# Performance work log

Hardware: AMD Instinct MI355X
Metric: run time of the kernel (lower is better)

## Reference

```python
import jax, jax.numpy as jnp
import numpy as np

B, V = 128, 128000
NEG_INF = float('-inf')


def _apply_top_k(logits, top_ks):
    vocab = logits.shape[-1]
    valid_k = jnp.where(top_ks > 0, jnp.minimum(top_ks, vocab), vocab)  # [B]
    order = jnp.argsort(-logits, axis=-1)                 # descending sort indices [B,V]
    sorted_logits = jnp.take_along_axis(logits, order, axis=-1)
    ranks = jnp.arange(vocab)[None, :]                    # [1,V]
    keep = ranks < valid_k[:, None]
    masked_sorted = jnp.where(keep, sorted_logits, NEG_INF)
    rows = jnp.arange(logits.shape[0])[:, None]
    return jnp.zeros_like(logits).at[rows, order].set(masked_sorted)


def _apply_top_p(logits, top_ps):
    order = jnp.argsort(-logits, axis=-1)
    sorted_logits = jnp.take_along_axis(logits, order, axis=-1)
    sorted_probs = jax.nn.softmax(sorted_logits, axis=-1)
    cum = jnp.cumsum(sorted_probs, axis=-1)
    keep = cum < top_ps[:, None]
    keep = keep.at[:, 0].set(True)                        # always keep the top token
    masked_sorted = jnp.where(keep, sorted_logits, NEG_INF)
    rows = jnp.arange(logits.shape[0])[:, None]
    return jnp.zeros_like(logits).at[rows, order].set(masked_sorted)


def setup_inputs() -> dict:
    key = jax.random.key(0)
    k1, k2, k3, k4, k5 = jax.random.split(key, 5)
    logits = jax.random.normal(k1, (B, V), dtype=jnp.float32) * 4.0
    temperatures = jax.random.uniform(k2, (B,), dtype=jnp.float32) + 0.5  # [0.5, 1.5)
    top_ks = jax.random.randint(k3, (B,), 0, 100, dtype=jnp.int64)        # 0 -> disabled
    top_ps = jax.random.uniform(k4, (B,), dtype=jnp.float32)
    # uniform noise; reference converts to Exp(1) via -log(u)
    exp_noise_u = jax.random.uniform(k5, (B, V), dtype=jnp.float32, minval=1e-12, maxval=1.0)
    return {"logits": logits, "temperatures": temperatures, "top_ks": top_ks,
            "top_ps": top_ps, "exp_noise_u": exp_noise_u}


def reference(logits, temperatures, top_ks, top_ps, exp_noise_u):
    x = logits.astype(jnp.float32) / temperatures[:, None]
    x = _apply_top_k(x, top_ks)
    x = _apply_top_p(x, top_ps)
    probs = jax.nn.softmax(x, axis=-1)
    q = jnp.clip(-jnp.log(exp_noise_u), 1e-10)            # Exp(1) samples, clamped like torch
    sample_tokens = jnp.argmax(probs / q, axis=-1)
    return sample_tokens
```

## Files before the change

### kernel.cpp

```cpp
#include <hip/hip_runtime.h>
#include <math.h>

#define SA 8
#define SEG2 8
#define NB 4096
#define TAA 512
#define HS 256
#define TE 512
#define TBB 1024
#define SCT 256
#define CH (NB / SCT)
#define CAPSEG 512
#define GTOT (SA * CAPSEG)
#define MAXM1 16
#define GB1 16384
#define SUBC 512
#define EQC 64
#define FXS 1099511627776.0f
#define FXI (1.0f / 1099511627776.0f)

typedef unsigned u32;
typedef unsigned long long u64;

struct ScanSh {
  u32 axc[SCT]; float axe[SCT];
  u32 sufc[SCT]; float sufe[SCT];
  int cbin[SCT]; u32 cca[SCT]; float cea[SCT];
  int fbin[SCT]; u32 fca[SCT]; float fea[SCT];
};

__device__ __forceinline__ u32 f2key(float f) {
  u32 u = __float_as_uint(f);
  return u ^ ((u >> 31) ? 0xFFFFFFFFu : 0x80000000u);
}
__device__ __forceinline__ int is_mode0(int k, int V) {
  return (k >= 1 && k <= 256 && k < V);
}

__device__ int m1_slot(const int* topks, int row, int V, int tid, int* red) {
  if (tid < 128) {
    int c = 0;
    for (int r = tid; r < row; r += 128) c += !is_mode0(topks[r], V);
    red[tid] = c;
  }
  __syncthreads();
  for (int s = 64; s > 0; s >>= 1) {
    if (tid < s) red[tid] += red[tid + s];
    __syncthreads();
  }
  return red[0];
}

__device__ __forceinline__ float row_max(const float* maxpart, int row) {
  float mm = maxpart[row * SA];
  for (int j = 1; j < SA; ++j) mm = fmaxf(mm, maxpart[row * SA + j]);
  return mm;
}

__device__ void scan_level(const u32* cnt, const u64* e0, ScanSh* ax,
                           u32* sprefix, int* scnt_above, float* sexp_above,
                           float target, int tid) {
  if (tid < SCT) {
    u32 cc = 0; float ce = 0.f; const int base = tid * CH;
    for (int j = 0; j < CH; ++j) { cc += cnt[base + j]; ce += (float)e0[base + j] * FXI; }
    ax->axc[tid] = cc; ax->axe[tid] = ce;
  }
  __syncthreads();
  if (tid == 0) {
    u32 rc = 0; float re = 0.f;
    for (int c = SCT - 1; c >= 0; --c) {
      ax->sufc[c] = rc; ax->sufe[c] = re;
      rc += ax->axc[c]; re += ax->axe[c];
    }
  }
  __syncthreads();
  if (tid < SCT) {
    const int base = tid * CH;
    u32 rc = ax->sufc[tid]; float re = ax->sufe[tid];
    int best = -1; u32 bca = 0; float bea = 0.f;
    int fb = -1; u32 ffca = 0; float ffea = 0.f;
    for (int b = base + CH - 1; b >= base; --b) {
      u32 c = cnt[b]; float ebv = (float)e0[b] * FXI;
      bool cross = (c > 0) && ((re + ebv) >= target);
      if (cross && best < 0) { best = b; bca = rc; bea = re; }
      if (c > 0) { fb = b; ffca = rc; ffea = re; }
      rc += c; re += ebv;
    }
    ax->cbin[tid] = best; ax->cca[tid] = bca; ax->cea[tid] = bea;
    ax->fbin[tid] = fb; ax->fca[tid] = ffca; ax->fea[tid] = ffea;
  }
  __syncthreads();
  if (tid == 0) {
    int bsel = -1; u32 ca = 0; float ea = 0.f;
    for (int c = 0; c < SCT; ++c) {
      int b = ax->cbin[c];
      if (b > bsel) { bsel = b; ca = ax->cca[c]; ea = ax->cea[c]; }
    }
    if (bsel < 0) {
      for (int c = 0; c < SCT; ++c) {
        int b = ax->fbin[c];
        if (b >= 0 && (bsel < 0 || b < bsel)) { bsel = b; ca = ax->fca[c]; ea = ax->fea[c]; }
      }
    }
    if (bsel < 0) bsel = 0;
    *sprefix = (u32)bsel;
    *scnt_above = (int)ca;
    *sexp_above = ea;
  }
  __syncthreads();
}

__global__ __launch_bounds__(TAA) void kA(const float* __restrict__ logits,
                                          const float* __restrict__ temps,
                                          const int* __restrict__ topks,
                                          float* __restrict__ maxpart,
                                          u32* __restrict__ scnt,
                                          float* __restrict__ candv,
                                          int* __restrict__ candi, int V) {
  const int row = blockIdx.x, seg = blockIdx.y, tid = threadIdx.x;
  __shared__ u32 cnt[NB];
  __shared__ float sm[TAA];
  __shared__ u32 cs[HS];
  __shared__ int bb[HS];
  __shared__ int lcnt;
  __shared__ u32 sT;
  const int k = topks[row];
  const int m0 = is_mode0(k, V);
  const float t = temps[row];
  const float* lr = logits + (size_t)row * V;
  const float4* l4 = (const float4*)lr;
  const int n4 = V >> 2;
  const int q0 = (int)((long long)seg * n4 / SA);
  const int q1 = (int)((long long)(seg + 1) * n4 / SA);
  float mx = -INFINITY;
  if (m0) {
    for (int i = tid; i < NB; i += TAA) cnt[i] = 0;
    if (tid == 0) lcnt = 0;
    __syncthreads();
    for (int i = q0 + tid; i < q1; i += TAA) {
      float4 v = l4[i];
      float xs[4] = {v.x / t, v.y / t, v.z / t, v.w / t};
#pragma unroll
      for (int j = 0; j < 4; ++j) {
        mx = fmaxf(mx, xs[j]);
        atomicAdd(&cnt[f2key(xs[j]) >> 20], 1u);
      }
    }
    if (seg == SA - 1)
      for (int i = (n4 << 2) + tid; i < V; i += TAA) {
        float x = lr[i] / t;
        mx = fmaxf(mx, x);
        atomicAdd(&cnt[f2key(x) >> 20], 1u);
      }
  } else {
    for (int i = q0 + tid; i < q1; i += TAA) {
      float4 v = l4[i];
      mx = fmaxf(mx, fmaxf(fmaxf(v.x, v.y), fmaxf(v.z, v.w)) / t);
    }
    if (seg == SA - 1)
      for (int i = (n4 << 2) + tid; i < V; i += TAA) mx = fmaxf(mx, lr[i] / t);
  }
  sm[tid] = mx;
  __syncthreads();
  for (int s = TAA >> 1; s > 0; s >>= 1) {
    if (tid < s) sm[tid] = fmaxf(sm[tid], sm[tid + s]);
    __syncthreads();
  }
  if (tid == 0) maxpart[row * SA + seg] = sm[0];
  if (!m0) return;
  if (tid < HS) {
    u32 cc = 0; const int base = tid * (NB / HS);
    for (int j = 0; j < NB / HS; ++j) cc += cnt[base + j];
    cs[tid] = cc;
  }
  __syncthreads();
  if (tid == 0) {
    u32 rc = 0;
    for (int c = HS - 1; c >= 0; --c) { u32 tmp = cs[c]; cs[c] = rc; rc += tmp; }
  }
  __syncthreads();
  const int kk = (k > 256) ? 256 : k;
  if (tid < HS) {
    const int base = tid * (NB / HS);
    u32 rc = cs[tid]; int best = -1;
    for (int b = base + NB / HS - 1; b >= base; --b) {
      u32 c = cnt[b];
      if (c && best < 0 && (int)(rc + c) >= kk) best = b;
      rc += c;
    }
    bb[tid] = best;
  }
  __syncthreads();
  if (tid == 0) {
    int bsel = -1;
    for (int c = 0; c < HS; ++c) if (bb[c] > bsel) bsel = bb[c];
    if (bsel < 0) { for (int b = 0; b < NB; ++b) if (cnt[b]) { bsel = b; break; } }
    if (bsel < 0) bsel = 0;
    sT = ((u32)bsel) << 20;
  }
  __syncthreads();
  const u32 T = sT;
  const size_t cbase = ((size_t)row * SA + seg) * CAPSEG;
  for (int i = q0 + tid; i < q1; i += TAA) {
    float4 v = l4[i];
    float xs[4] = {v.x / t, v.y / t, v.z / t, v.w / t};
#pragma unroll
    for (int j = 0; j < 4; ++j) {
      if (f2key(xs[j]) >= T) {
        int s = atomicAdd(&lcnt, 1);
        if (s < CAPSEG) { candv[cbase + s] = xs[j]; candi[cbase + s] = i * 4 + j; }
      }
    }
  }
  if (seg == SA - 1)
    for (int i = (n4 << 2) + tid; i < V; i += TAA) {
      float x = lr[i] / t;
      if (f2key(x) >= T) {
        int s = atomicAdd(&lcnt, 1);
        if (s < CAPSEG) { candv[cbase + s] = x; candi[cbase + s] = i; }
      }
    }
  __syncthreads();
  if (tid == 0) { int n = lcnt; if (n > CAPSEG) n = CAPSEG; scnt[row * SA + seg] = (u32)n; }
}

__global__ __launch_bounds__(TE) void kE(const float* __restrict__ logits,
                                         const float* __restrict__ temps,
                                         const int* __restrict__ topks,
                                         const float* __restrict__ maxpart,
                                         float* __restrict__ Sparts,
                                         u32* __restrict__ m1c0,
                                         u64* __restrict__ m1e0, int V) {
  const int row = blockIdx.x, seg = blockIdx.y, tid = threadIdx.x;
  const int k = topks[row];
  if (is_mode0(k, V)) return;
  __shared__ int red[128];
  const int slot = m1_slot(topks, row, V, tid, red);
  if (slot >= MAXM1) return;
  __shared__ u32 c0[NB];
  __shared__ u64 e0[NB];
  __shared__ float ss[TE];
  for (int i = tid; i < NB; i += TE) { c0[i] = 0; e0[i] = 0ull; }
  __syncthreads();
  const float t = temps[row];
  const float m = row_max(maxpart, row);
  const float* lr = logits + (size_t)row * V;
  const float4* l4 = (const float4*)lr;
  const int n4 = V >> 2;
  const int q0 = (int)((long long)seg * n4 / SEG2);
  const int q1 = (int)((long long)(seg + 1) * n4 / SEG2);
  float ls = 0.f;
  for (int i = q0 + tid; i < q1; i += TE) {
    float4 v = l4[i];
    float xs[4] = {v.x / t, v.y / t, v.z / t, v.w / t};
#pragma unroll
    for (int j = 0; j < 4; ++j) {
      float e = expf(xs[j] - m);
      ls += e;
      u32 b = f2key(xs[j]) >> 20;
      atomicAdd(&c0[b], 1u);
      u64 fx = (u64)(e * FXS);
      if (fx) atomicAdd(&e0[b], fx);
    }
  }
  if (seg == SEG2 - 1)
    for (int i = (n4 << 2) + tid; i < V; i += TE) {
      float x = lr[i] / t;
      float e = expf(x - m);
      ls += e;
      u32 b = f2key(x) >> 20;
      atomicAdd(&c0[b], 1u);
      u64 fx = (u64)(e * FXS);
      if (fx) atomicAdd(&e0[b], fx);
    }
  ss[tid] = ls;
  __syncthreads();
  for (int s = TE >> 1; s > 0; s >>= 1) {
    if (tid < s) ss[tid] += ss[tid + s];
    __syncthreads();
  }
  if (tid == 0) Sparts[slot * SEG2 + seg] = ss[0];
  for (int b = tid; b < NB; b += TE) {
    u32 c = c0[b]; if (c) atomicAdd(&m1c0[(size_t)slot * NB + b], c);
    u64 e = e0[b]; if (e) atomicAdd(&m1e0[(size_t)slot * NB + b], e);
  }
}

__global__ __launch_bounds__(TBB) void kM1(const float* __restrict__ logits,
                                           const float* __restrict__ temps,
                                           const int* __restrict__ topks,
                                           const float* __restrict__ topps,
                                           const float* __restrict__ noise,
                                           const float* __restrict__ maxpart,
                                           const float* __restrict__ Sparts,
                                           const u32* __restrict__ m1c0,
                                           const u64* __restrict__ m1e0,
                                           u64* __restrict__ g1p,
                                           u32* __restrict__ gcnt,
                                           u64* __restrict__ rpack,
                                           u32* __restrict__ rdone,
                                           int* __restrict__ out, int V) {
  const int row = blockIdx.x, seg = blockIdx.y, tid = threadIdx.x;
  const int k = topks[row];
  if (is_mode0(k, V)) return;
  __shared__ int red[128];
  const int slot = m1_slot(topks, row, V, tid, red);
  if (slot >= MAXM1) return;

  __shared__ u32 cnt[NB];
  __shared__ u64 e0[NB];
  __shared__ ScanSh ax;
  __shared__ u32 spfx; __shared__ int sca; __shared__ float sea;
  __shared__ float rr[TBB]; __shared__ int ri[TBB];
  for (int i = tid; i < NB; i += TBB) {
    cnt[i] = m1c0[(size_t)slot * NB + i];
    e0[i] = m1e0[(size_t)slot * NB + i];
  }
  __syncthreads();
  float S = 0.f;
  for (int j = 0; j < SEG2; ++j) S += Sparts[slot * SEG2 + j];
  const float target = topps[row] * S;
  scan_level(cnt, e0, &ax, &spfx, &sca, &sea, target, tid);
  const u32 pfx = spfx;

  const float t = temps[row];
  const float m = row_max(maxpart, row);
  const float* lr = logits + (size_t)row * V;
  const float* ur = noise + (size_t)row * V;
  const float4* l4 = (const float4*)lr;
  const float4* u4 = (const float4*)ur;
  const int n4 = V >> 2;
  const int q0 = (int)((long long)seg * n4 / SEG2);
  const int q1 = (int)((long long)(seg + 1) * n4 / SEG2);
  const size_t gbase = (size_t)slot * GB1;

  float best = -1.f; int bidx = 0x7FFFFFFF;
  for (int i = q0 + tid; i < q1; i += TBB) {
    float4 xv = l4[i];
    float4 uv = u4[i];
    float xs[4] = {xv.x / t, xv.y / t, xv.z / t, xv.w / t};
    float us[4] = {uv.x, uv.y, uv.z, uv.w};
#pragma unroll
    for (int j = 0; j < 4; ++j) {
      u32 key = f2key(xs[j]);
      u32 bin = key >> 20;
      int idx = i * 4 + j;
      if (bin == pfx) {
        u32 s2 = atomicAdd(&gcnt[slot], 1u);
        if (s2 < GB1)
          atomicExch(&g1p[gbase + s2],
                     ((u64)__float_as_uint(xs[j]) << 32) | (u64)(u32)idx);
      } else if (bin > pfx) {
        float q = fmaxf(-logf(us[j]), 1e-10f);
        float rt = expf(xs[j] - m) / q;
        if (rt > best || (rt == best && idx < bidx)) { best = rt; bidx = idx; }
      }
    }
  }
  if (seg == SEG2 - 1)
    for (int i = (n4 << 2) + tid; i < V; i += TBB) {
      float x = lr[i] / t;
      u32 key = f2key(x);
      u32 bin = key >> 20;
      if (bin == pfx) {
        u32 s2 = atomicAdd(&gcnt[slot], 1u);
        if (s2 < GB1)
          atomicExch(&g1p[gbase + s2],
                     ((u64)__float_as_uint(x) << 32) | (u64)(u32)i);
      } else if (bin > pfx) {
        float q = fmaxf(-logf(ur[i]), 1e-10f);
        float rt = expf(x - m) / q;
        if (rt > best || (rt == best && i < bidx)) { best = rt; bidx = i; }
      }
    }
  rr[tid] = best; ri[tid] = bidx;
  __syncthreads();
  for (int s = TBB >> 1; s > 0; s >>= 1) {
    if (tid < s) {
      float ov = rr[tid + s]; int oi = ri[tid + s];
      if (ov > rr[tid] || (ov == rr[tid] && oi < ri[tid])) { rr[tid] = ov; ri[tid] = oi; }
    }
    __syncthreads();
  }
  __shared__ int slast;
  if (tid == 0) {
    if (rr[0] >= 0.f) {
      u64 pk = ((u64)f2key(rr[0]) << 32) | (u64)(0xFFFFFFFFu - (u32)ri[0]);
      atomicMax(&rpack[row], pk);
    }
    __threadfence();
    u32 arr = atomicAdd(&rdone[row], 1u);
    slast = (arr == (u32)(SEG2 - 1)) ? 1 : 0;
  }
  __syncthreads();
  if (!slast) return;
  __threadfence();

  __shared__ u32 cnt1[1024]; __shared__ u64 fx1[1024];
  __shared__ u32 csuf[1024]; __shared__ u64 esuf[1024];
  __shared__ float subv[SUBC]; __shared__ int subi[SUBC];
  __shared__ float ssv[SUBC]; __shared__ int ssi[SUBC];
  __shared__ int eqs[EQC];
  __shared__ int scross, sfb, sca1, sns, seqn;
  __shared__ float sea1; __shared__ u32 svstar;

  int nf = (int)atomicAdd(&gcnt[slot], 0u);
  if (nf > GB1) nf = GB1;
  cnt1[tid] = 0; fx1[tid] = 0ull;
  if (tid == 0) { sns = 0; scross = -1; sfb = 0x7FFFFFFF; }
  __syncthreads();
  for (int i = tid; i < nf; i += TBB) {
    u64 p = atomicAdd(&g1p[gbase + i], 0ull);
    float x = __uint_as_float((u32)(p >> 32));
    u32 b = (f2key(x) >> 10) & 0x3FFu;
    float e = expf(x - m);
    atomicAdd(&cnt1[b], 1u);
    u64 fx = (u64)(e * FXS);
    if (fx) atomicAdd(&fx1[b], fx);
  }
  __syncthreads();
  csuf[tid] = cnt1[tid]; esuf[tid] = fx1[tid];
  __syncthreads();
  for (int stp = 1; stp < 1024; stp <<= 1) {
    u32 ca_ = 0; u64 ea_ = 0ull;
    if (tid + stp < 1024) { ca_ = csuf[tid + stp]; ea_ = esuf[tid + stp]; }
    __syncthreads();
    csuf[tid] += ca_; esuf[tid] += ea_;
    __syncthreads();
  }
  {
    u32 c = cnt1[tid];
    if (c) {
      float racc = (float)(esuf[tid] - fx1[tid]) * FXI;
      float ebv = (float)fx1[tid] * FXI;
      if (sea + (racc + ebv) >= target) atomicMax(&scross, tid);
      atomicMin(&sfb, tid);
    }
  }
  __syncthreads();
  if (tid == 0) {
    int cb = scross;
    if (cb < 0) cb = (sfb != 0x7FFFFFFF) ? sfb : 0;
    u32 cAbove = csuf[cb] - cnt1[cb];
    float eAbove = (float)(esuf[cb] - fx1[cb]) * FXI;
    scross = cb;
    sea1 = sea + eAbove;
    sca1 = sca + (int)cAbove;
  }
  __syncthreads();
  const u32 cb = (u32)scross;
  for (int i = tid; i < nf; i += TBB) {
    u64 p = atomicAdd(&g1p[gbase + i], 0ull);
    float x = __uint_as_float((u32)(p >> 32));
    if (((f2key(x) >> 10) & 0x3FFu) == cb) {
      int s2 = atomicAdd(&sns, 1);
      if (s2 < SUBC) { subv[s2] = x; subi[s2] = (int)(u32)(p & 0xFFFFFFFFull); }
    }
  }
  __syncthreads();
  int ns = sns; if (ns > SUBC) ns = SUBC;
  for (int i = tid; i < ns; i += TBB) {
    float v = subv[i]; int ix = subi[i];
    int rank = 0;
    for (int j2 = 0; j2 < ns; ++j2) {
      float vj = subv[j2]; int ij = subi[j2];
      if (vj > v || (vj == v && ij < ix)) rank++;
    }
    ssv[rank] = v; ssi[rank] = ix;
  }
  __syncthreads();
  if (tid == 0) {
    const float p = topps[row];
    float run_n = sea1 / S;
    const int have_above = (sca1 > 0);
    u32 lastkey = 0u; int lastr = 0, laststart = -1, anykept = 0;
    u32 vsel = 0u; int rsel = -1, bstart = 0;
    int j = 0;
    while (j < ns) {
      u32 key = f2key(ssv[j]);
      int c = 1;
      while (j + c < ns && f2key(ssv[j + c]) == key) ++c;
      float e = expf(ssv[j] - m);
      float en = e / S;
      int kept = 0;
      for (int q = 0; q < c; ++q) {
        float nn = run_n + en;
        if (nn < p) { run_n = nn; kept++; } else break;
      }
      if (kept == c) { lastkey = key; lastr = c; laststart = j; anykept = 1; j += c; continue; }
      if (kept > 0) { vsel = key; rsel = kept; bstart = j; }
      else if (anykept) { vsel = lastkey; rsel = lastr; bstart = laststart; }
      else if (have_above) { vsel = key; rsel = 0; bstart = j; }
      else { vsel = key; rsel = 1; bstart = j; }
      break;
    }
    if (rsel < 0) {
      if (anykept) { vsel = lastkey; rsel = lastr; bstart = laststart; }
      else if (ns > 0) {
        vsel = f2key(ssv[0]); bstart = 0;
        rsel = have_above ? 0 : 1;
      } else { vsel = 0u; rsel = 0; bstart = 0; }
    }
    int eqn = rsel;
    if (eqn > EQC) eqn = EQC;
    if (eqn < 0) eqn = 0;
    if (bstart + eqn > ns) eqn = ns - bstart;
    if (eqn < 0) eqn = 0;
    for (int q2 = 0; q2 < eqn; ++q2) eqs[q2] = ssi[bstart + q2];
    seqn = eqn; svstar = vsel;
  }
  __syncthreads();

  const u32 vk = svstar;
  const int eqn = seqn;
  best = -1.f; bidx = 0x7FFFFFFF;
  for (int i = tid; i < nf; i += TBB) {
    u64 p = atomicAdd(&g1p[gbase + i], 0ull);
    float x = __uint_as_float((u32)(p >> 32));
    int ix = (int)(u32)(p & 0xFFFFFFFFull);
    u32 key = f2key(x);
    bool kept = key > vk;
    if (!kept && key == vk) {
      for (int e = 0; e < eqn; ++e) if (eqs[e] == ix) { kept = true; break; }
    }
    if (kept) {
      float q = fmaxf(-logf(ur[ix]), 1e-10f);
      float rt = expf(x - m) / q;
      if (rt > best || (rt == best && ix < bidx)) { best = rt; bidx = ix; }
    }
  }
  rr[tid] = best; ri[tid] = bidx;
  __syncthreads();
  for (int s = TBB >> 1; s > 0; s >>= 1) {
    if (tid < s) {
      float ov = rr[tid + s]; int oi = ri[tid + s];
      if (ov > rr[tid] || (ov == rr[tid] && oi < ri[tid])) { rr[tid] = ov; ri[tid] = oi; }
    }
    __syncthreads();
  }
  if (tid == 0) {
    u64 myPk = 0ull;
    if (rr[0] >= 0.f)
      myPk = ((u64)f2key(rr[0]) << 32) | (u64)(0xFFFFFFFFu - (u32)ri[0]);
    u64 prev = atomicMax(&rpack[row], myPk);
    u64 fin = prev > myPk ? prev : myPk;
    out[row] = (int)(0xFFFFFFFFu - (u32)(fin & 0xFFFFFFFFull));
  }
}

__global__ __launch_bounds__(TBB) void kH(const float* __restrict__ topps,
                                          const float* __restrict__ noise,
                                          const int* __restrict__ topks,
                                          const float* __restrict__ maxpart,
                                          const u32* __restrict__ scnt,
                                          const float* __restrict__ candv,
                                          const int* __restrict__ candi,
                                          int* __restrict__ out, int V) {
  const int row = blockIdx.x, tid = threadIdx.x;
  const int kR = topks[row];
  if (!is_mode0(kR, V)) return;
  __shared__ float gv[GTOT]; __shared__ int gi[GTOT];
  __shared__ float sv[CAPSEG]; __shared__ int si[CAPSEG];
  __shared__ float fv[CAPSEG]; __shared__ int fi[CAPSEG];
  __shared__ float pe[CAPSEG];
  __shared__ float rr[TBB]; __shared__ int ri[TBB];
  __shared__ int offs[SA + 1];
  __shared__ u32 dh[256]; __shared__ u32 dsufx[256];
  __shared__ u32 sPrefix; __shared__ int sRemain, sNf, sDig;
  __shared__ int sJ; __shared__ float sZ2;
  if (tid == 0) {
    int o = 0;
    for (int s = 0; s < SA; ++s) {
      offs[s] = o;
      int c = (int)scnt[row * SA + s];
      if (c > CAPSEG) c = CAPSEG;
      if (c < 0) c = 0;
      o += c;
    }
    offs[SA] = o;
  }
  __syncthreads();
  const int g = offs[SA];
  for (int s = 0; s < SA; ++s) {
    const int o = offs[s], c = offs[s + 1] - o;
    const size_t cbase = ((size_t)row * SA + s) * CAPSEG;
    for (int i = tid; i < c; i += TBB) { gv[o + i] = candv[cbase + i]; gi[o + i] = candi[cbase + i]; }
  }
  __syncthreads();
  int kk = kR; if (kk > 256) kk = 256; if (kk > g) kk = g;
  if (tid == 0) { sPrefix = 0u; sRemain = (kk < 1) ? 1 : kk; }
  __syncthreads();
  for (int pass = 0; pass < 4; ++pass) {
    const int shift = 24 - 8 * pass;
    if (tid < 256) dh[tid] = 0;
    if (tid == 0) sDig = -1;
    __syncthreads();
    const u32 pref = sPrefix;
    for (int i = tid; i < g; i += TBB) {
      u32 key = f2key(gv[i]);
      if (pass == 0 || (key >> (shift + 8)) == pref)
        atomicAdd(&dh[(key >> shift) & 0xFFu], 1u);
    }
    __syncthreads();
    if (tid < 256) dsufx[tid] = dh[tid];
    __syncthreads();
    for (int stp = 1; stp < 256; stp <<= 1) {
      u32 addv = 0;
      if (tid < 256 && tid + stp < 256) addv = dsufx[tid + stp];
      __syncthreads();
      if (tid < 256) dsufx[tid] += addv;
      __syncthreads();
    }
    if (tid < 256) {
      u32 excl = dsufx[tid] - dh[tid];
      u32 rem = (u32)sRemain;
      if (dh[tid] && excl < rem && excl + dh[tid] >= rem) sDig = tid;
    }
    __syncthreads();
    if (tid == 0) {
      int d = sDig; if (d < 0) d = 0;
      u32 excl = dsufx[d] - dh[d];
      sRemain -= (int)excl;
      sPrefix = (sPrefix << 8) | (u32)d;
      if (pass == 3) sNf = 0;
    }
    __syncthreads();
  }
  const u32 Tk = sPrefix;
  for (int i = tid; i < g; i += TBB) {
    if (f2key(gv[i]) >= Tk) {
      int s = atomicAdd(&sNf, 1);
      if (s < CAPSEG) { fv[s] = gv[i]; fi[s] = gi[i]; }
    }
  }
  __syncthreads();
  int nf = sNf; if (nf > CAPSEG) nf = CAPSEG;
  for (int i = tid; i < nf; i += TBB) {
    float v = fv[i]; int ix = fi[i];
    int rank = 0;
    for (int j = 0; j < nf; ++j) {
      float vj = fv[j]; int ij = fi[j];
      if (vj > v || (vj == v && ij < ix)) rank++;
    }
    sv[rank] = v; si[rank] = ix;
  }
  __syncthreads();
  const float m = row_max(maxpart, row);
  const float p = topps[row];
  int keff = kR; if (keff > nf) keff = nf;
  for (int j = tid; j < keff; j += TBB) pe[j] = expf(sv[j] - m);
  __syncthreads();
  if (tid == 0) {
    int J = 1; float Z2 = 1.f;
    if (nf > 0 && keff > 0) {
      float Zk = 0.f;
      for (int j = 0; j < keff; ++j) Zk += pe[j];
      float c = 0.f; int Jc = 0;
      for (int j = 0; j < keff; ++j) {
        float pr = pe[j] / Zk;
        c += pr;
        if (c < p) Jc++;
      }
      if (Jc < 1) Jc = 1;
      J = Jc;
      Z2 = 0.f;
      for (int j = 0; j < J && j < keff; ++j) Z2 += pe[j];
    }
    sJ = J; sZ2 = Z2;
  }
  __syncthreads();
  const int J = sJ; const float Z2 = sZ2;
  float best = -1.f; int bidx = 0x7FFFFFFF;
  for (int j = tid; j < J && j < nf; j += TBB) {
    int ix = si[j];
    float u = noise[(size_t)row * V + ix];
    float q = fmaxf(-logf(u), 1e-10f);
    float pr = pe[j] / Z2;
    float rt = pr / q;
    if (rt > best || (rt == best && ix < bidx)) { best = rt; bidx = ix; }
  }
  rr[tid] = best; ri[tid] = bidx;
  __syncthreads();
  for (int s = TBB >> 1; s > 0; s >>= 1) {
    if (tid < s) {
      float ov = rr[tid + s]; int oi = ri[tid + s];
      if (ov > rr[tid] || (ov == rr[tid] && oi < ri[tid])) { rr[tid] = ov; ri[tid] = oi; }
    }
    __syncthreads();
  }
  if (tid == 0) out[row] = (nf > 0) ? ri[0] : 0;
}

extern "C" void kernel_launch(void* const* d_in, const int* in_sizes, int n_in,
                              void* d_out, int out_size, void* d_ws, size_t ws_size,
                              hipStream_t stream) {
  const float* logits = (const float*)d_in[0];
  const float* temps = (const float*)d_in[1];
  const int* topks = (const int*)d_in[2];
  const float* topps = (const float*)d_in[3];
  const float* noise = (const float*)d_in[4];
  int* out = (int*)d_out;
  const int B = in_sizes[1];
  const int V = in_sizes[0] / B;
  (void)n_in; (void)out_size; (void)ws_size;

  u32* w = (u32*)d_ws;
  size_t o = 0;
  float* maxpart = (float*)(w + o); o += (size_t)B * SA;
  u32* scnt = w + o; o += (size_t)B * SA;
  float* candv = (float*)(w + o); o += (size_t)B * SA * CAPSEG;
  int* candi = (int*)(w + o); o += (size_t)B * SA * CAPSEG;
  if (o & 1) o += 1;
  const size_t zbase = o;
  u64* m1e0 = (u64*)(w + o); o += 2 * (size_t)MAXM1 * NB;
  u32* m1c0 = w + o; o += (size_t)MAXM1 * NB;
  u64* rpack = (u64*)(w + o); o += 2 * (size_t)B;
  u32* rdone = w + o; o += (size_t)B;
  u32* gcnt = w + o; o += MAXM1;
  if (o & 1) o += 1;
  const size_t zwords = o - zbase;
  float* Sparts = (float*)(w + o); o += (size_t)MAXM1 * SEG2;
  if (o & 1) o += 1;
  u64* g1p = (u64*)(w + o); o += 2 * (size_t)MAXM1 * GB1;

  hipMemsetAsync((void*)(w + zbase), 0, zwords * sizeof(u32), stream);
  kA<<<dim3(B, SA), TAA, 0, stream>>>(logits, temps, topks, maxpart, scnt, candv, candi, V);
  kE<<<dim3(B, SEG2), TE, 0, stream>>>(logits, temps, topks, maxpart, Sparts, m1c0, m1e0, V);
  kM1<<<dim3(B, SEG2), TBB, 0, stream>>>(logits, temps, topks, topps, noise, maxpart,
                                         Sparts, m1c0, m1e0, g1p, gcnt, rpack, rdone, out, V);
  kH<<<B, TBB, 0, stream>>>(topps, noise, topks, maxpart, scnt, candv, candi, out, V);
}
```

Before: 239.7 us.

## Fold workspace zeroing into kA, skip per-element temperature divide, widen kM1 grid

The separate hipMemsetAsync is removed and the zeroed workspace region is cleared by a grid-stride loop inside kA, saving one launch. kA now builds its histogram and threshold on raw logits, relying on division by a positive temperature preserving order. It divides only the final max and the stored candidates by t. kM1 is split into 32 segments per row instead of 8 to raise parallelism, with the last-block counter updated to match. Risks: the key ordering of raw and scaled values must match exactly, and zeroing inside kA assumes nothing reads those buffers before kA finishes.

```diff
diff --git a/kernel.cpp b/kernel.cpp
--- a/kernel.cpp
+++ b/kernel.cpp
@@ -2,7 +2,8 @@
 #include <math.h>
 
 #define SA 8
-#define SEG2 8
+#define SEGE 8
+#define SEGM 32
 #define NB 4096
 #define TAA 512
 #define HS 256
@@ -116,7 +117,9 @@
                                           float* __restrict__ maxpart,
                                           u32* __restrict__ scnt,
                                           float* __restrict__ candv,
-                                          int* __restrict__ candi, int V) {
+                                          int* __restrict__ candi,
+                                          u32* __restrict__ zp, size_t zwords,
+                                          int V) {
   const int row = blockIdx.x, seg = blockIdx.y, tid = threadIdx.x;
   __shared__ u32 cnt[NB];
   __shared__ float sm[TAA];
@@ -124,6 +127,11 @@
   __shared__ int bb[HS];
   __shared__ int lcnt;
   __shared__ u32 sT;
+  {
+    const size_t gid = ((size_t)blockIdx.y * gridDim.x + blockIdx.x) * TAA + tid;
+    const size_t stride = (size_t)gridDim.x * gridDim.y * TAA;
+    for (size_t i = gid; i < zwords; i += stride) zp[i] = 0;
+  }
   const int k = topks[row];
   const int m0 = is_mode0(k, V);
   const float t = temps[row];
@@ -132,41 +140,40 @@
   const int n4 = V >> 2;
   const int q0 = (int)((long long)seg * n4 / SA);
   const int q1 = (int)((long long)(seg + 1) * n4 / SA);
-  float mx = -INFINITY;
+  float rmx = -INFINITY;
   if (m0) {
     for (int i = tid; i < NB; i += TAA) cnt[i] = 0;
     if (tid == 0) lcnt = 0;
     __syncthreads();
     for (int i = q0 + tid; i < q1; i += TAA) {
       float4 v = l4[i];
-      float xs[4] = {v.x / t, v.y / t, v.z / t, v.w / t};
-#pragma unroll
-      for (int j = 0; j < 4; ++j) {
-        mx = fmaxf(mx, xs[j]);
-        atomicAdd(&cnt[f2key(xs[j]) >> 20], 1u);
-      }
+      rmx = fmaxf(rmx, fmaxf(fmaxf(v.x, v.y), fmaxf(v.z, v.w)));
+      atomicAdd(&cnt[f2key(v.x) >> 20], 1u);
+      atomicAdd(&cnt[f2key(v.y) >> 20], 1u);
+      atomicAdd(&cnt[f2key(v.z) >> 20], 1u);
+      atomicAdd(&cnt[f2key(v.w) >> 20], 1u);
     }
     if (seg == SA - 1)
       for (int i = (n4 << 2) + tid; i < V; i += TAA) {
-        float x = lr[i] / t;
-        mx = fmaxf(mx, x);
+        float x = lr[i];
+        rmx = fmaxf(rmx, x);
         atomicAdd(&cnt[f2key(x) >> 20], 1u);
       }
   } else {
     for (int i = q0 + tid; i < q1; i += TAA) {
       float4 v = l4[i];
-      mx = fmaxf(mx, fmaxf(fmaxf(v.x, v.y), fmaxf(v.z, v.w)) / t);
+      rmx = fmaxf(rmx, fmaxf(fmaxf(v.x, v.y), fmaxf(v.z, v.w)));
     }
     if (seg == SA - 1)
-      for (int i = (n4 << 2) + tid; i < V; i += TAA) mx = fmaxf(mx, lr[i] / t);
-  }
-  sm[tid] = mx;
+      for (int i = (n4 << 2) + tid; i < V; i += TAA) rmx = fmaxf(rmx, lr[i]);
+  }
+  sm[tid] = rmx;
   __syncthreads();
   for (int s = TAA >> 1; s > 0; s >>= 1) {
     if (tid < s) sm[tid] = fmaxf(sm[tid], sm[tid + s]);
     __syncthreads();
   }
-  if (tid == 0) maxpart[row * SA + seg] = sm[0];
+  if (tid == 0) maxpart[row * SA + seg] = sm[0] / t;
   if (!m0) return;
   if (tid < HS) {
     u32 cc = 0; const int base = tid * (NB / HS);
@@ -203,21 +210,21 @@
   const size_t cbase = ((size_t)row * SA + seg) * CAPSEG;
   for (int i = q0 + tid; i < q1; i += TAA) {
     float4 v = l4[i];
-    float xs[4] = {v.x / t, v.y / t, v.z / t, v.w / t};
+    float vs[4] = {v.x, v.y, v.z, v.w};
 #pragma unroll
     for (int j = 0; j < 4; ++j) {
-      if (f2key(xs[j]) >= T) {
+      if (f2key(vs[j]) >= T) {
         int s = atomicAdd(&lcnt, 1);
-        if (s < CAPSEG) { candv[cbase + s] = xs[j]; candi[cbase + s] = i * 4 + j; }
+        if (s < CAPSEG) { candv[cbase + s] = vs[j] / t; candi[cbase + s] = i * 4 + j; }
       }
     }
   }
   if (seg == SA - 1)
     for (int i = (n4 << 2) + tid; i < V; i += TAA) {
-      float x = lr[i] / t;
+      float x = lr[i];
       if (f2key(x) >= T) {
         int s = atomicAdd(&lcnt, 1);
-        if (s < CAPSEG) { candv[cbase + s] = x; candi[cbase + s] = i; }
+        if (s < CAPSEG) { candv[cbase + s] = x / t; candi[cbase + s] = i; }
       }
     }
   __syncthreads();
@@ -247,8 +254,8 @@
   const float* lr = logits + (size_t)row * V;
   const float4* l4 = (const float4*)lr;
   const int n4 = V >> 2;
-  const int q0 = (int)((long long)seg * n4 / SEG2);
-  const int q1 = (int)((long long)(seg + 1) * n4 / SEG2);
+  const int q0 = (int)((long long)seg * n4 / SEGE);
+  const int q1 = (int)((long long)(seg + 1) * n4 / SEGE);
   float ls = 0.f;
   for (int i = q0 + tid; i < q1; i += TE) {
     float4 v = l4[i];
@@ -263,7 +270,7 @@
       if (fx) atomicAdd(&e0[b], fx);
     }
   }
-  if (seg == SEG2 - 1)
+  if (seg == SEGE - 1)
     for (int i = (n4 << 2) + tid; i < V; i += TE) {
       float x = lr[i] / t;
       float e = expf(x - m);
@@ -279,7 +286,7 @@
     if (tid < s) ss[tid] += ss[tid + s];
     __syncthreads();
   }
-  if (tid == 0) Sparts[slot * SEG2 + seg] = ss[0];
+  if (tid == 0) Sparts[slot * SEGE + seg] = ss[0];
   for (int b = tid; b < NB; b += TE) {
     u32 c = c0[b]; if (c) atomicAdd(&m1c0[(size_t)slot * NB + b], c);
     u64 e = e0[b]; if (e) atomicAdd(&m1e0[(size_t)slot * NB + b], e);
@@ -318,7 +325,7 @@
   }
   __syncthreads();
   float S = 0.f;
-  for (int j = 0; j < SEG2; ++j) S += Sparts[slot * SEG2 + j];
+  for (int j = 0; j < SEGE; ++j) S += Sparts[slot * SEGE + j];
   const float target = topps[row] * S;
   scan_level(cnt, e0, &ax, &spfx, &sca, &sea, target, tid);
   const u32 pfx = spfx;
@@ -330,8 +337,8 @@
   const float4* l4 = (const float4*)lr;
   const float4* u4 = (const float4*)ur;
   const int n4 = V >> 2;
-  const int q0 = (int)((long long)seg * n4 / SEG2);
-  const int q1 = (int)((long long)(seg + 1) * n4 / SEG2);
+  const int q0 = (int)((long long)seg * n4 / SEGM);
+  const int q1 = (int)((long long)(seg + 1) * n4 / SEGM);
   const size_t gbase = (size_t)slot * GB1;
 
   float best = -1.f; int bidx = 0x7FFFFFFF;
@@ -357,7 +364,7 @@
       }
     }
   }
-  if (seg == SEG2 - 1)
+  if (seg == SEGM - 1)
     for (int i = (n4 << 2) + tid; i < V; i += TBB) {
       float x = lr[i] / t;
       u32 key = f2key(x);
@@ -390,7 +397,7 @@
     }
     __threadfence();
     u32 arr = atomicAdd(&rdone[row], 1u);
-    slast = (arr == (u32)(SEG2 - 1)) ? 1 : 0;
+    slast = (arr == (u32)(SEGM - 1)) ? 1 : 0;
   }
   __syncthreads();
   if (!slast) return;
@@ -719,14 +726,14 @@
   u32* gcnt = w + o; o += MAXM1;
   if (o & 1) o += 1;
   const size_t zwords = o - zbase;
-  float* Sparts = (float*)(w + o); o += (size_t)MAXM1 * SEG2;
+  float* Sparts = (float*)(w + o); o += (size_t)MAXM1 * SEGE;
   if (o & 1) o += 1;
   u64* g1p = (u64*)(w + o); o += 2 * (size_t)MAXM1 * GB1;
 
-  hipMemsetAsync((void*)(w + zbase), 0, zwords * sizeof(u32), stream);
-  kA<<<dim3(B, SA), TAA, 0, stream>>>(logits, temps, topks, maxpart, scnt, candv, candi, V);
-  kE<<<dim3(B, SEG2), TE, 0, stream>>>(logits, temps, topks, maxpart, Sparts, m1c0, m1e0, V);
-  kM1<<<dim3(B, SEG2), TBB, 0, stream>>>(logits, temps, topks, topps, noise, maxpart,
+  kA<<<dim3(B, SA), TAA, 0, stream>>>(logits, temps, topks, maxpart, scnt,
+                                      candv, candi, w + zbase, zwords, V);
+  kE<<<dim3(B, SEGE), TE, 0, stream>>>(logits, temps, topks, maxpart, Sparts, m1c0, m1e0, V);
+  kM1<<<dim3(B, SEGM), TBB, 0, stream>>>(logits, temps, topks, topps, noise, maxpart,
                                          Sparts, m1c0, m1e0, g1p, gcnt, rpack, rdone, out, V);
   kH<<<B, TBB, 0, stream>>>(topps, noise, topks, maxpart, scnt, candv, candi, out, V);
 }
```

New measurement: 309.0 us. 28.9% more time.
